# Optimization experiments

Measured on AMD Instinct MI355X. Metric: run time of the kernel, lower is better.

Reference implementation:

```python
import jax, jax.numpy as jnp
import numpy as np

B, S, D, H = 4, 1024, 2048, 16
DH = D // H          # head_dim = 128
EPS = 1e-6           # equinox nn.RMSNorm default eps


def setup_inputs() -> dict:
    ks = jax.random.split(jax.random.key(0), 8)
    return {
        "x": jax.random.normal(ks[0], (B, S, D), jnp.float32),
        # Flux-style rope table, broadcast over heads: (B, S, 1, d_head/2, 2, 2)
        "pe": jax.random.normal(ks[1], (B, S, 1, DH // 2, 2, 2), jnp.float32),
        "w_qkv": jax.random.normal(ks[2], (D, 3 * D), jnp.float32) * (1.0 / np.sqrt(D)),
        "w_o": jax.random.normal(ks[3], (D, D), jnp.float32) * (1.0 / np.sqrt(D)),
        "q_scale": 1.0 + 0.02 * jax.random.normal(ks[4], (DH,), jnp.float32),
        "q_bias": 0.02 * jax.random.normal(ks[5], (DH,), jnp.float32),
        "k_scale": 1.0 + 0.02 * jax.random.normal(ks[6], (DH,), jnp.float32),
        "k_bias": 0.02 * jax.random.normal(ks[7], (DH,), jnp.float32),
    }


def reference(x, pe, w_qkv, w_o, q_scale, q_bias, k_scale, k_bias):
    b, s, dm = x.shape
    # fused QKV projection -> (B, S, 3, H, DH); rearrange '(qkv heads dim)'
    qkv = (x @ w_qkv).reshape(b, s, 3, H, DH)
    q, k, v = qkv[:, :, 0], qkv[:, :, 1], qkv[:, :, 2]

    # per-head RMSNorm (QKNorm), eqx: w * (x / rms) + b
    def rms(u, scale, bias):
        inv = jax.lax.rsqrt(jnp.mean(u * u, axis=-1, keepdims=True) + EPS)
        return u * inv * scale + bias

    q = rms(q, q_scale, q_bias)
    k = rms(k, k_scale, k_bias)

    # RoPE: view last dim as (DH//2, 1, 2) pairs, apply 2x2 rotation from pe
    def rope(u):
        u2 = u.reshape(b, s, H, DH // 2, 1, 2)
        r = pe[..., 0] * u2[..., 0] + pe[..., 1] * u2[..., 1]  # (B,S,H,DH//2,2)
        return r.reshape(b, s, H, DH)

    q = rope(q)
    k = rope(k)

    # non-causal SDPA, layout (B, T, N, H), default scale 1/sqrt(DH)
    attn = jax.nn.dot_product_attention(q, k, v)
    return attn.reshape(b, s, dm) @ w_o
```

## Files before the change

### kernel.cpp

```cpp
#include <hip/hip_runtime.h>
#include <hip/hip_bf16.h>

typedef _Float16 f16_t;
typedef _Float16 f16x2 __attribute__((ext_vector_type(2)));
typedef _Float16 f16x4 __attribute__((ext_vector_type(4)));
typedef _Float16 f16x8 __attribute__((ext_vector_type(8)));
typedef float f32x4 __attribute__((ext_vector_type(4)));

#define GLOAD_LDS16(gp, lp)                                                        \
  __builtin_amdgcn_global_load_lds(                                                \
      (const __attribute__((address_space(1))) void*)(gp),                         \
      (__attribute__((address_space(3))) void*)(lp), 16, 0, 0)

template<int N> __device__ __forceinline__ void vmwait() {
    if constexpr (N >= 12)     asm volatile("s_waitcnt vmcnt(12)" ::: "memory");
    else if constexpr (N == 9) asm volatile("s_waitcnt vmcnt(9)" ::: "memory");
    else if constexpr (N == 8) asm volatile("s_waitcnt vmcnt(8)" ::: "memory");
    else if constexpr (N == 6) asm volatile("s_waitcnt vmcnt(6)" ::: "memory");
    else if constexpr (N == 4) asm volatile("s_waitcnt vmcnt(4)" ::: "memory");
    else if constexpr (N == 3) asm volatile("s_waitcnt vmcnt(3)" ::: "memory");
    else                       asm volatile("s_waitcnt vmcnt(0)" ::: "memory");
}

__global__ __launch_bounds__(256) void conv_f16(const float* __restrict__ in,
                                                f16_t* __restrict__ out)
{
    int i = blockIdx.x * 256 + threadIdx.x;
    float4 a = *(const float4*)&in[(size_t)i * 8];
    float4 b = *(const float4*)&in[(size_t)i * 8 + 4];
    f16x8 o = {(f16_t)a.x, (f16_t)a.y, (f16_t)a.z, (f16_t)a.w,
               (f16_t)b.x, (f16_t)b.y, (f16_t)b.z, (f16_t)b.w};
    *(f16x8*)&out[(size_t)i * 8] = o;
}

__global__ __launch_bounds__(256) void transpose_f16(const float* __restrict__ in,
                                                     f16_t* __restrict__ out,
                                                     int R, int C)
{
    __shared__ float t[32][33];
    const int tr = blockIdx.y, tc = blockIdx.x;
    const int r = threadIdx.x >> 3, c4 = (threadIdx.x & 7) * 4;
    float4 v = *(const float4*)&in[(size_t)(tr * 32 + r) * C + tc * 32 + c4];
    t[r][c4 + 0] = v.x; t[r][c4 + 1] = v.y; t[r][c4 + 2] = v.z; t[r][c4 + 3] = v.w;
    __syncthreads();
    f16x4 o = {(f16_t)t[c4 + 0][r], (f16_t)t[c4 + 1][r],
               (f16_t)t[c4 + 2][r], (f16_t)t[c4 + 3][r]};
    *(f16x4*)&out[(size_t)(tc * 32 + r) * R + tr * 32 + c4] = o;
}

template<int BN, int WMC, int WNC, int F16OUT>
__global__ __launch_bounds__(512, 2) void gemm_v3(const f16_t* __restrict__ A,
                                                  const f16_t* __restrict__ BT,
                                                  void* __restrict__ Cout,
                                                  int M, int N, int K, int gx)
{
    extern __shared__ char smem[];
    constexpr int WMT = 256 / WMC, WNT = BN / WNC;
    constexpr int MF = WMT / 16, NF = WNT / 16, MFH = MF / 2;
    constexpr int BNL = BN / 128;
    constexpr int L = 2 + BNL;

    const int tid = threadIdx.x, lane = tid & 63, wave = tid >> 6;
    const int lh = lane >> 4, li = lane & 15;
    const int wr = wave / WNC, wc = wave % WNC;

    const int nwg = gridDim.x, bid = blockIdx.x;
    const int swz = (bid & 7) * (nwg >> 3) + (bid >> 3);
    const int bx = swz % gx, by = swz / gx;

    const size_t bmK = (size_t)(by * 256) * K;
    const size_t bnK = (size_t)(bx * BN) * K;
    const int NT = K >> 5;

    f32x4 acc[MF][NF];
#pragma unroll
    for (int i = 0; i < MF; ++i)
#pragma unroll
        for (int j = 0; j < NF; ++j) acc[i][j] = (f32x4){0.f, 0.f, 0.f, 0.f};

#define STAGE(t)                                                                   \
    do {                                                                           \
        const int buf_ = (t) & 3;                                                  \
        const int kof_ = (t) << 5;                                                 \
        char* Ab_ = smem + buf_ * 16384;                                           \
        char* Bb_ = smem + 65536 + buf_ * (BN * 64);                               \
        _Pragma("unroll")                                                          \
        for (int i_ = 0; i_ < 2; ++i_) {                                           \
            const int c_ = i_ * 512 + tid;                                         \
            const int row_ = c_ >> 2;                                              \
            const int gu_ = (c_ & 3) ^ ((row_ >> 1) & 3);                          \
            GLOAD_LDS16(A + bmK + (size_t)row_ * K + kof_ + gu_ * 8,               \
                        Ab_ + (i_ * 512 + wave * 64) * 16);                        \
        }                                                                          \
        _Pragma("unroll")                                                          \
        for (int i_ = 0; i_ < BNL; ++i_) {                                         \
            const int c_ = i_ * 512 + tid;                                         \
            const int row_ = c_ >> 2;                                              \
            const int gu_ = (c_ & 3) ^ ((row_ >> 1) & 3);                          \
            GLOAD_LDS16(BT + bnK + (size_t)row_ * K + kof_ + gu_ * 8,              \
                        Bb_ + (i_ * 512 + wave * 64) * 16);                        \
        }                                                                          \
    } while (0)

    STAGE(0); STAGE(1); STAGE(2); STAGE(3);

    const int runit = (lh ^ ((li >> 1) & 3)) << 3;

    for (int t = 0; t < NT; ++t) {
        if (t + 3 < NT)      vmwait<3 * L>();
        else if (t + 2 < NT) vmwait<2 * L>();
        else if (t + 1 < NT) vmwait<L>();
        else                 vmwait<0>();
        __builtin_amdgcn_s_barrier();
        __builtin_amdgcn_sched_barrier(0);

        const f16_t* Ab = (const f16_t*)(smem + (t & 3) * 16384);
        const f16_t* Bb = (const f16_t*)(smem + 65536 + (t & 3) * (BN * 64));

        f16x8 af[MFH], bf[NF];
#pragma unroll
        for (int j = 0; j < MFH; ++j)
            af[j] = *(const f16x8*)(Ab + (wr * WMT + j * 16 + li) * 32 + runit);
#pragma unroll
        for (int nf = 0; nf < NF; ++nf)
            bf[nf] = *(const f16x8*)(Bb + (wc * WNT + nf * 16 + li) * 32 + runit);
        __builtin_amdgcn_s_setprio(1);
#pragma unroll
        for (int j = 0; j < MFH; ++j)
#pragma unroll
            for (int nf = 0; nf < NF; ++nf)
                acc[j][nf] = __builtin_amdgcn_mfma_f32_16x16x32_f16(af[j], bf[nf],
                                                                    acc[j][nf], 0, 0, 0);
        __builtin_amdgcn_s_setprio(0);
        __builtin_amdgcn_sched_barrier(0);
#pragma unroll
        for (int j = 0; j < MFH; ++j)
            af[j] = *(const f16x8*)(Ab + (wr * WMT + (MFH + j) * 16 + li) * 32 + runit);
        __builtin_amdgcn_s_setprio(1);
#pragma unroll
        for (int j = 0; j < MFH; ++j)
#pragma unroll
            for (int nf = 0; nf < NF; ++nf)
                acc[MFH + j][nf] = __builtin_amdgcn_mfma_f32_16x16x32_f16(af[j], bf[nf],
                                                                          acc[MFH + j][nf],
                                                                          0, 0, 0);
        __builtin_amdgcn_s_setprio(0);
        __builtin_amdgcn_sched_barrier(0);

        __builtin_amdgcn_s_barrier();
        if (t + 4 < NT) STAGE(t + 4);
        __builtin_amdgcn_sched_barrier(0);
    }
#undef STAGE

#pragma unroll
    for (int mf = 0; mf < MF; ++mf)
#pragma unroll
        for (int nf = 0; nf < NF; ++nf)
#pragma unroll
            for (int r = 0; r < 4; ++r) {
                const int row = by * 256 + wr * WMT + mf * 16 + lh * 4 + r;
                const int col = bx * BN + wc * WNT + nf * 16 + li;
                if (F16OUT)
                    ((f16_t*)Cout)[(size_t)row * N + col] = (f16_t)acc[mf][nf][r];
                else
                    ((float*)Cout)[(size_t)row * N + col] = acc[mf][nf][r];
            }
}

__global__ __launch_bounds__(256) void rmsrope_f16(f16_t* __restrict__ qkv,
                                                   const float* __restrict__ pe,
                                                   const float* __restrict__ qs,
                                                   const float* __restrict__ qb,
                                                   const float* __restrict__ ks,
                                                   const float* __restrict__ kb)
{
    const int unit = blockIdx.x * 4 + (threadIdx.x >> 6);
    const int l = threadIdx.x & 63;
    const int bs = unit >> 5, h = (unit >> 1) & 15, comp = unit & 1;
    f16_t* base = qkv + ((size_t)bs * 3 + comp) * 2048 + h * 128;
    const float* sc = comp ? ks : qs;
    const float* bi = comp ? kb : qb;

    f16x2 u = *(const f16x2*)(base + 2 * l);
    float u0 = (float)u[0], u1 = (float)u[1];
    float ss = u0 * u0 + u1 * u1;
#pragma unroll
    for (int o = 32; o; o >>= 1) ss += __shfl_xor(ss, o);
    float inv = rsqrtf(ss * (1.f / 128.f) + 1e-6f);

    float2 scv = *(const float2*)(sc + 2 * l);
    float2 biv = *(const float2*)(bi + 2 * l);
    float a = u0 * inv * scv.x + biv.x;
    float c = u1 * inv * scv.y + biv.y;
    float4 p4 = *(const float4*)(pe + (size_t)bs * 256 + l * 4);
    f16x2 o = {(f16_t)(p4.x * a + p4.y * c), (f16_t)(p4.z * a + p4.w * c)};
    *(f16x2*)(base + 2 * l) = o;
}

__global__ __launch_bounds__(256) void attn_f16(const f16_t* __restrict__ qkv,
                                                f16_t* __restrict__ out)
{
    __shared__ f16_t Kl[2][64 * 128];
    __shared__ f16_t Vt[128 * 72];
    const int tid = threadIdx.x, lane = tid & 63, wave = tid >> 6;
    const int lh = lane >> 4, li = lane & 15;
    const int bidx = blockIdx.x;
    const int bh = bidx & 63;
    const int qt = bidx >> 6;
    const int h = bh & 15, b = bh >> 4;
    const size_t seqbase = (size_t)b * 1024;
    const float SCALE = 0.08838834764831845f;

    const int qbase = qt * 128 + wave * 32;
    f16x8 qreg[2][4];
#pragma unroll
    for (int qf = 0; qf < 2; ++qf) {
        const f16_t* qp = qkv + (seqbase + qbase + qf * 16 + li) * 6144 + h * 128;
#pragma unroll
        for (int c = 0; c < 4; ++c) {
            f16x8 v = *(const f16x8*)(qp + c * 32 + lh * 8);
#pragma unroll
            for (int j = 0; j < 8; ++j) v[j] = (f16_t)((float)v[j] * SCALE);
            qreg[qf][c] = v;
        }
    }

    f32x4 oacc[2][8];
#pragma unroll
    for (int qf = 0; qf < 2; ++qf)
#pragma unroll
        for (int dt = 0; dt < 8; ++dt) oacc[qf][dt] = (f32x4){0.f, 0.f, 0.f, 0.f};
    float mrun[2] = {-1e30f, -1e30f}, lrun[2] = {0.f, 0.f};

    const int vd0 = (tid & 31) * 4;
    const int vk0 = (tid >> 5) * 8;
    f16x4 vreg[8];

#define STAGE_K(t, buf)                                                            \
    do {                                                                           \
        _Pragma("unroll")                                                          \
        for (int it = 0; it < 4; ++it) {                                           \
            const int c_ = it * 256 + tid;                                         \
            const int row_ = c_ >> 4, cc_ = c_ & 15;                               \
            const f16_t* src_ = qkv + (seqbase + (t) * 64 + row_) * 6144 + 2048 +  \
                                h * 128 + ((cc_ ^ (row_ & 7)) << 3);               \
            GLOAD_LDS16(src_, (char*)&Kl[buf][0] + (it * 256 + wave * 64) * 16);   \
        }                                                                          \
    } while (0)

#define LOAD_V(t)                                                                  \
    do {                                                                           \
        _Pragma("unroll")                                                          \
        for (int r_ = 0; r_ < 8; ++r_)                                             \
            vreg[r_] = *(const f16x4*)(qkv + (seqbase + (t) * 64 + vk0 + r_) *     \
                                       6144 + 4096 + h * 128 + vd0);               \
    } while (0)

    STAGE_K(0, 0);
    LOAD_V(0);

    for (int t = 0; t < 16; ++t) {
        const int buf = t & 1;
        __syncthreads();

#pragma unroll
        for (int dd = 0; dd < 4; ++dd) {
            f16x8 w;
#pragma unroll
            for (int r = 0; r < 8; ++r) w[r] = vreg[r][dd];
            *(f16x8*)&Vt[(vd0 + dd) * 72 + vk0] = w;
        }
        __syncthreads();

        if (t < 15) {
            STAGE_K(t + 1, buf ^ 1);
            LOAD_V(t + 1);
        }

        float s[2][16];
#pragma unroll
        for (int kvt = 0; kvt < 4; ++kvt) {
            f32x4 a0 = (f32x4){0.f, 0.f, 0.f, 0.f}, a1 = a0;
#pragma unroll
            for (int c = 0; c < 4; ++c) {
                const int kvrow = kvt * 16 + li;
                f16x8 kf = *(const f16x8*)&Kl[buf][kvrow * 128 +
                                                   (((c * 4 + lh) ^ (li & 7)) << 3)];
                a0 = __builtin_amdgcn_mfma_f32_16x16x32_f16(kf, qreg[0][c], a0, 0, 0, 0);
                a1 = __builtin_amdgcn_mfma_f32_16x16x32_f16(kf, qreg[1][c], a1, 0, 0, 0);
            }
#pragma unroll
            for (int r = 0; r < 4; ++r) { s[0][kvt * 4 + r] = a0[r]; s[1][kvt * 4 + r] = a1[r]; }
        }

        float pmax[2];
#pragma unroll
        for (int qf = 0; qf < 2; ++qf) {
            float mx = s[qf][0];
#pragma unroll
            for (int i = 1; i < 16; ++i) mx = fmaxf(mx, s[qf][i]);
            mx = fmaxf(mx, __shfl_xor(mx, 16));
            mx = fmaxf(mx, __shfl_xor(mx, 32));
            pmax[qf] = mx;
        }
        const bool defer = __all((pmax[0] - mrun[0] <= 8.f) && (pmax[1] - mrun[1] <= 8.f));
        if (!defer) {
#pragma unroll
            for (int qf = 0; qf < 2; ++qf) {
                const float mn = fmaxf(mrun[qf], pmax[qf]);
                const float alpha = __expf(mrun[qf] - mn);
                lrun[qf] *= alpha;
                mrun[qf] = mn;
                float ar[4];
#pragma unroll
                for (int r = 0; r < 4; ++r) ar[r] = __shfl(alpha, 4 * lh + r);
#pragma unroll
                for (int dt = 0; dt < 8; ++dt)
#pragma unroll
                    for (int r = 0; r < 4; ++r) oacc[qf][dt][r] *= ar[r];
            }
        }

        f16x8 pa[2][2];
#pragma unroll
        for (int qf = 0; qf < 2; ++qf) {
            float ls = 0.f;
            float p[16];
#pragma unroll
            for (int i = 0; i < 16; ++i) { p[i] = __expf(s[qf][i] - mrun[qf]); ls += p[i]; }
            ls += __shfl_xor(ls, 16);
            ls += __shfl_xor(ls, 32);
            lrun[qf] += ls;
#pragma unroll
            for (int hf = 0; hf < 2; ++hf)
#pragma unroll
                for (int j = 0; j < 8; ++j)
                    pa[qf][hf][j] = (f16_t)p[(2 * hf + (j >> 2)) * 4 + (j & 3)];
        }

#pragma unroll
        for (int dt = 0; dt < 8; ++dt) {
            const int drow = dt * 16 + li;
            f16x4 v0 = *(const f16x4*)&Vt[drow * 72 + 4 * lh];
            f16x4 v1 = *(const f16x4*)&Vt[drow * 72 + 16 + 4 * lh];
            f16x4 v2 = *(const f16x4*)&Vt[drow * 72 + 32 + 4 * lh];
            f16x4 v3 = *(const f16x4*)&Vt[drow * 72 + 48 + 4 * lh];
            f16x8 vf0 = {v0[0], v0[1], v0[2], v0[3], v1[0], v1[1], v1[2], v1[3]};
            f16x8 vf1 = {v2[0], v2[1], v2[2], v2[3], v3[0], v3[1], v3[2], v3[3]};
#pragma unroll
            for (int qf = 0; qf < 2; ++qf) {
                oacc[qf][dt] = __builtin_amdgcn_mfma_f32_16x16x32_f16(pa[qf][0], vf0,
                                                                      oacc[qf][dt], 0, 0, 0);
                oacc[qf][dt] = __builtin_amdgcn_mfma_f32_16x16x32_f16(pa[qf][1], vf1,
                                                                      oacc[qf][dt], 0, 0, 0);
            }
        }
    }

#pragma unroll
    for (int qf = 0; qf < 2; ++qf) {
        const float inv = 1.f / lrun[qf];
        float ir[4];
#pragma unroll
        for (int r = 0; r < 4; ++r) ir[r] = __shfl(inv, 4 * lh + r);
#pragma unroll
        for (int dt = 0; dt < 8; ++dt)
#pragma unroll
            for (int r = 0; r < 4; ++r) {
                const int row = qbase + qf * 16 + 4 * lh + r;
                out[(seqbase + row) * 2048 + h * 128 + dt * 16 + li] =
                    (f16_t)(oacc[qf][dt][r] * ir[r]);
            }
    }
#undef STAGE_K
#undef LOAD_V
}

extern "C" void kernel_launch(void* const* d_in, const int* in_sizes, int n_in,
                              void* d_out, int out_size, void* d_ws, size_t ws_size,
                              hipStream_t stream) {
    const float* x       = (const float*)d_in[0];
    const float* pe      = (const float*)d_in[1];
    const float* w_qkv   = (const float*)d_in[2];
    const float* w_o     = (const float*)d_in[3];
    const float* q_scale = (const float*)d_in[4];
    const float* q_bias  = (const float*)d_in[5];
    const float* k_scale = (const float*)d_in[6];
    const float* k_bias  = (const float*)d_in[7];
    float* out = (float*)d_out;

    char* ws = (char*)d_ws;
    f16_t* x16    = (f16_t*)(ws);
    f16_t* wqkvT  = (f16_t*)(ws + 16777216);
    f16_t* woT    = (f16_t*)(ws + 41943040);
    f16_t* qkv16  = (f16_t*)(ws + 50331648);
    f16_t* attn16 = (f16_t*)(ws + 100663296);

    hipFuncSetAttribute((const void*)&gemm_v3<256, 2, 4, 1>,
                        hipFuncAttributeMaxDynamicSharedMemorySize, 131072);
    hipFuncSetAttribute((const void*)&gemm_v3<128, 4, 2, 0>,
                        hipFuncAttributeMaxDynamicSharedMemorySize, 98304);

    conv_f16<<<4096, 256, 0, stream>>>(x, x16);
    transpose_f16<<<dim3(6144 / 32, 2048 / 32), 256, 0, stream>>>(w_qkv, wqkvT, 2048, 6144);
    transpose_f16<<<dim3(2048 / 32, 2048 / 32), 256, 0, stream>>>(w_o, woT, 2048, 2048);

    gemm_v3<256, 2, 4, 1><<<384, 512, 131072, stream>>>(x16, wqkvT, qkv16,
                                                        4096, 6144, 2048, 24);

    rmsrope_f16<<<32768, 256, 0, stream>>>(qkv16, pe, q_scale, q_bias, k_scale, k_bias);

    attn_f16<<<512, 256, 0, stream>>>(qkv16, attn16);

    gemm_v3<128, 4, 2, 0><<<256, 512, 98304, stream>>>(attn16, woT, out,
                                                       4096, 2048, 2048, 16);
}
```

Baseline: 309.0 us.

## Retile GEMMs to one wave and use triple-buffered single-barrier pipeline

The templated GEMM gets new tile shapes: 256x384 for the QKV projection and 128x256 for the output projection. Each now launches exactly 256 workgroups, which avoids a partial second wave on the 384-block QKV launch. The 4-stage double-barrier prefetch loop becomes a 3-buffer ring that prefetches two tiles ahead right after a single barrier per K-step, and the MFMA inner loop is split into A/B halves to limit live fragment registers. The trade-offs are a shallower prefetch depth, which may expose global-load latency, and larger per-wave accumulator footprints.

After: 278.2 us. 10.0% less time.

```diff
diff --git a/kernel.cpp b/kernel.cpp
--- a/kernel.cpp
+++ b/kernel.cpp
@@ -13,12 +13,10 @@
       (__attribute__((address_space(3))) void*)(lp), 16, 0, 0)
 
 template<int N> __device__ __forceinline__ void vmwait() {
-    if constexpr (N >= 12)     asm volatile("s_waitcnt vmcnt(12)" ::: "memory");
-    else if constexpr (N == 9) asm volatile("s_waitcnt vmcnt(9)" ::: "memory");
-    else if constexpr (N == 8) asm volatile("s_waitcnt vmcnt(8)" ::: "memory");
+    if constexpr (N == 0)      asm volatile("s_waitcnt vmcnt(0)" ::: "memory");
+    else if constexpr (N == 3) asm volatile("s_waitcnt vmcnt(3)" ::: "memory");
+    else if constexpr (N == 5) asm volatile("s_waitcnt vmcnt(5)" ::: "memory");
     else if constexpr (N == 6) asm volatile("s_waitcnt vmcnt(6)" ::: "memory");
-    else if constexpr (N == 4) asm volatile("s_waitcnt vmcnt(4)" ::: "memory");
-    else if constexpr (N == 3) asm volatile("s_waitcnt vmcnt(3)" ::: "memory");
     else                       asm volatile("s_waitcnt vmcnt(0)" ::: "memory");
 }
 
@@ -48,27 +46,28 @@
     *(f16x4*)&out[(size_t)(tc * 32 + r) * R + tr * 32 + c4] = o;
 }
 
-template<int BN, int WMC, int WNC, int F16OUT>
-__global__ __launch_bounds__(512, 2) void gemm_v3(const f16_t* __restrict__ A,
+template<int BM, int BN, int GY, int F16OUT>
+__global__ __launch_bounds__(512, 2) void gemm_v4(const f16_t* __restrict__ A,
                                                   const f16_t* __restrict__ BT,
                                                   void* __restrict__ Cout,
-                                                  int M, int N, int K, int gx)
+                                                  int M, int N, int K)
 {
     extern __shared__ char smem[];
-    constexpr int WMT = 256 / WMC, WNT = BN / WNC;
-    constexpr int MF = WMT / 16, NF = WNT / 16, MFH = MF / 2;
-    constexpr int BNL = BN / 128;
-    constexpr int L = 2 + BNL;
+    constexpr int WMT = BM / 2, WNT = BN / 4;
+    constexpr int MF = WMT / 16, NF = WNT / 16, MFH = MF / 2, NFH = NF / 2;
+    constexpr int ALI = BM / 128, BLI = BN / 128;
+    constexpr int L = ALI + BLI;
+    constexpr int ABUFB = BM * 64, BBUFB = BN * 64;
 
     const int tid = threadIdx.x, lane = tid & 63, wave = tid >> 6;
     const int lh = lane >> 4, li = lane & 15;
-    const int wr = wave / WNC, wc = wave % WNC;
+    const int wr = wave >> 2, wc = wave & 3;
 
     const int nwg = gridDim.x, bid = blockIdx.x;
     const int swz = (bid & 7) * (nwg >> 3) + (bid >> 3);
-    const int bx = swz % gx, by = swz / gx;
-
-    const size_t bmK = (size_t)(by * 256) * K;
+    const int by = swz % GY, bx = swz / GY;
+
+    const size_t bmK = (size_t)(by * BM) * K;
     const size_t bnK = (size_t)(bx * BN) * K;
     const int NT = K >> 5;
 
@@ -78,14 +77,13 @@
 #pragma unroll
         for (int j = 0; j < NF; ++j) acc[i][j] = (f32x4){0.f, 0.f, 0.f, 0.f};
 
-#define STAGE(t)                                                                   \
+#define STAGE(t, b)                                                                \
     do {                                                                           \
-        const int buf_ = (t) & 3;                                                  \
         const int kof_ = (t) << 5;                                                 \
-        char* Ab_ = smem + buf_ * 16384;                                           \
-        char* Bb_ = smem + 65536 + buf_ * (BN * 64);                               \
+        char* Ab_ = smem + (b) * ABUFB;                                            \
+        char* Bb_ = smem + 3 * ABUFB + (b) * BBUFB;                                \
         _Pragma("unroll")                                                          \
-        for (int i_ = 0; i_ < 2; ++i_) {                                           \
+        for (int i_ = 0; i_ < ALI; ++i_) {                                         \
             const int c_ = i_ * 512 + tid;                                         \
             const int row_ = c_ >> 2;                                              \
             const int gu_ = (c_ & 3) ^ ((row_ >> 1) & 3);                          \
@@ -93,7 +91,7 @@
                         Ab_ + (i_ * 512 + wave * 64) * 16);                        \
         }                                                                          \
         _Pragma("unroll")                                                          \
-        for (int i_ = 0; i_ < BNL; ++i_) {                                         \
+        for (int i_ = 0; i_ < BLI; ++i_) {                                         \
             const int c_ = i_ * 512 + tid;                                         \
             const int row_ = c_ >> 2;                                              \
             const int gu_ = (c_ & 3) ^ ((row_ >> 1) & 3);                          \
@@ -102,54 +100,50 @@
         }                                                                          \
     } while (0)
 
-    STAGE(0); STAGE(1); STAGE(2); STAGE(3);
+    STAGE(0, 0);
+    STAGE(1, 1);
 
     const int runit = (lh ^ ((li >> 1) & 3)) << 3;
 
+    int rb = 0;
     for (int t = 0; t < NT; ++t) {
-        if (t + 3 < NT)      vmwait<3 * L>();
-        else if (t + 2 < NT) vmwait<2 * L>();
-        else if (t + 1 < NT) vmwait<L>();
-        else                 vmwait<0>();
+        if (t + 1 < NT) vmwait<L>();
+        else            vmwait<0>();
         __builtin_amdgcn_s_barrier();
+        if (t + 2 < NT) {
+            const int sb = rb ? rb - 1 : 2;
+            STAGE(t + 2, sb);
+        }
         __builtin_amdgcn_sched_barrier(0);
 
-        const f16_t* Ab = (const f16_t*)(smem + (t & 3) * 16384);
-        const f16_t* Bb = (const f16_t*)(smem + 65536 + (t & 3) * (BN * 64));
-
-        f16x8 af[MFH], bf[NF];
-#pragma unroll
-        for (int j = 0; j < MFH; ++j)
-            af[j] = *(const f16x8*)(Ab + (wr * WMT + j * 16 + li) * 32 + runit);
-#pragma unroll
-        for (int nf = 0; nf < NF; ++nf)
-            bf[nf] = *(const f16x8*)(Bb + (wc * WNT + nf * 16 + li) * 32 + runit);
-        __builtin_amdgcn_s_setprio(1);
-#pragma unroll
-        for (int j = 0; j < MFH; ++j)
-#pragma unroll
-            for (int nf = 0; nf < NF; ++nf)
-                acc[j][nf] = __builtin_amdgcn_mfma_f32_16x16x32_f16(af[j], bf[nf],
-                                                                    acc[j][nf], 0, 0, 0);
-        __builtin_amdgcn_s_setprio(0);
-        __builtin_amdgcn_sched_barrier(0);
-#pragma unroll
-        for (int j = 0; j < MFH; ++j)
-            af[j] = *(const f16x8*)(Ab + (wr * WMT + (MFH + j) * 16 + li) * 32 + runit);
-        __builtin_amdgcn_s_setprio(1);
-#pragma unroll
-        for (int j = 0; j < MFH; ++j)
-#pragma unroll
-            for (int nf = 0; nf < NF; ++nf)
-                acc[MFH + j][nf] = __builtin_amdgcn_mfma_f32_16x16x32_f16(af[j], bf[nf],
-                                                                          acc[MFH + j][nf],
-                                                                          0, 0, 0);
-        __builtin_amdgcn_s_setprio(0);
-        __builtin_amdgcn_sched_barrier(0);
-
-        __builtin_amdgcn_s_barrier();
-        if (t + 4 < NT) STAGE(t + 4);
-        __builtin_amdgcn_sched_barrier(0);
+        const f16_t* Ab = (const f16_t*)(smem + rb * ABUFB);
+        const f16_t* Bb = (const f16_t*)(smem + 3 * ABUFB + rb * BBUFB);
+        f16x8 af[MFH], bf[NFH];
+#pragma unroll
+        for (int bh = 0; bh < 2; ++bh) {
+#pragma unroll
+            for (int j = 0; j < NFH; ++j)
+                bf[j] = *(const f16x8*)(Bb + (wc * WNT + (bh * NFH + j) * 16 + li) * 32
+                                        + runit);
+#pragma unroll
+            for (int ah = 0; ah < 2; ++ah) {
+#pragma unroll
+                for (int j = 0; j < MFH; ++j)
+                    af[j] = *(const f16x8*)(Ab + (wr * WMT + (ah * MFH + j) * 16 + li) * 32
+                                            + runit);
+                __builtin_amdgcn_s_setprio(1);
+#pragma unroll
+                for (int i = 0; i < MFH; ++i)
+#pragma unroll
+                    for (int j = 0; j < NFH; ++j)
+                        acc[ah * MFH + i][bh * NFH + j] =
+                            __builtin_amdgcn_mfma_f32_16x16x32_f16(
+                                af[i], bf[j], acc[ah * MFH + i][bh * NFH + j], 0, 0, 0);
+                __builtin_amdgcn_s_setprio(0);
+                __builtin_amdgcn_sched_barrier(0);
+            }
+        }
+        rb = (rb == 2) ? 0 : rb + 1;
     }
 #undef STAGE
 
@@ -159,7 +153,7 @@
         for (int nf = 0; nf < NF; ++nf)
 #pragma unroll
             for (int r = 0; r < 4; ++r) {
-                const int row = by * 256 + wr * WMT + mf * 16 + lh * 4 + r;
+                const int row = by * BM + wr * WMT + mf * 16 + lh * 4 + r;
                 const int col = bx * BN + wc * WNT + nf * 16 + li;
                 if (F16OUT)
                     ((f16_t*)Cout)[(size_t)row * N + col] = (f16_t)acc[mf][nf][r];
@@ -397,22 +391,22 @@
     f16_t* qkv16  = (f16_t*)(ws + 50331648);
     f16_t* attn16 = (f16_t*)(ws + 100663296);
 
-    hipFuncSetAttribute((const void*)&gemm_v3<256, 2, 4, 1>,
-                        hipFuncAttributeMaxDynamicSharedMemorySize, 131072);
-    hipFuncSetAttribute((const void*)&gemm_v3<128, 4, 2, 0>,
-                        hipFuncAttributeMaxDynamicSharedMemorySize, 98304);
+    hipFuncSetAttribute((const void*)&gemm_v4<256, 384, 16, 1>,
+                        hipFuncAttributeMaxDynamicSharedMemorySize, 122880);
+    hipFuncSetAttribute((const void*)&gemm_v4<128, 256, 32, 0>,
+                        hipFuncAttributeMaxDynamicSharedMemorySize, 73728);
 
     conv_f16<<<4096, 256, 0, stream>>>(x, x16);
     transpose_f16<<<dim3(6144 / 32, 2048 / 32), 256, 0, stream>>>(w_qkv, wqkvT, 2048, 6144);
     transpose_f16<<<dim3(2048 / 32, 2048 / 32), 256, 0, stream>>>(w_o, woT, 2048, 2048);
 
-    gemm_v3<256, 2, 4, 1><<<384, 512, 131072, stream>>>(x16, wqkvT, qkv16,
-                                                        4096, 6144, 2048, 24);
+    gemm_v4<256, 384, 16, 1><<<256, 512, 122880, stream>>>(x16, wqkvT, qkv16,
+                                                           4096, 6144, 2048);
 
     rmsrope_f16<<<32768, 256, 0, stream>>>(qkv16, pe, q_scale, q_bias, k_scale, k_bias);
 
     attn_f16<<<512, 256, 0, stream>>>(qkv16, attn16);
 
-    gemm_v3<128, 4, 2, 0><<<256, 512, 98304, stream>>>(attn16, woT, out,
-                                                       4096, 2048, 2048, 16);
-}
+    gemm_v4<128, 256, 32, 0><<<256, 512, 73728, stream>>>(attn16, woT, out,
+                                                          4096, 2048, 2048);
+}
```
